# Optimization experiments

Measured on AMD Instinct MI355X. Metric: run time of the kernel, lower is better.

## Reference

```python
import jax, jax.numpy as jnp
import numpy as np

T = 0.07          # cfg.CAP.TEMP
K = 50            # cfg.CAP.HARD_NEG_K
LOSS_WEIGHT = 0.5 # cfg.CAP.LOSS_WEIGHT
C_CAM = 8         # number of cameras
P = 2048          # pseudo-ID classes per camera bank


def setup_inputs() -> dict:
    key = jax.random.key(0)
    k1, k2, k3, k4 = jax.random.split(key, 4)
    B, D = 256, 2048
    inputs = jax.random.normal(k1, (B, D), jnp.float32)
    labels = jax.random.randint(k2, (B,), 0, P)
    cams = jax.random.randint(k3, (B,), 0, C_CAM)
    tempV = jax.random.normal(k4, (C_CAM * P, D), jnp.float32)
    tempV = tempV / jnp.linalg.norm(tempV, axis=1, keepdims=True)  # memory rows are L2-normalized
    return {"inputs": inputs, "labels": labels, "cams": cams, "tempV": tempV}


def _seg_mean_sum(vals, cams):
    # original loops over unique cams: loss += mean(vals within cam); empty cams contribute 0
    sums = jax.ops.segment_sum(vals, cams, num_segments=C_CAM)
    cnts = jax.ops.segment_sum(jnp.ones_like(vals), cams, num_segments=C_CAM)
    return jnp.sum(jnp.where(cnts > 0, sums / jnp.maximum(cnts, 1.0), 0.0))


def reference(inputs, labels, cams, tempV):
    B = inputs.shape[0]
    # cfg.CAP.NORM_FEAT
    x = inputs / jnp.linalg.norm(inputs, axis=1, keepdims=True)

    # one fused matmul against the concatenated memory; per-camera banks are contiguous P-slices
    all_logits = x @ tempV.T                      # [B, C_CAM*P]
    logits3 = all_logits.reshape(B, C_CAM, P)

    # ---- intra-camera loss: logits against the sample's own camera bank ----
    percam = jnp.take_along_axis(logits3, cams[:, None, None], axis=1)[:, 0, :] / T  # [B, P]
    lse_i = jax.scipy.special.logsumexp(percam, axis=1)
    ce = lse_i - jnp.take_along_axis(percam, labels[:, None], axis=1)[:, 0]
    loss_intra = _seg_mean_sum(ce, cams)

    # ---- inter-camera loss with hard-negative mining ----
    rows = jnp.arange(B)[:, None]
    # each ID has one centroid in every camera bank: positions label + P*cam
    ori_ind = labels[:, None] + P * jnp.arange(C_CAM)[None, :]        # [B, C_CAM]
    sims = all_logits.at[rows, ori_ind].set(-10000.0)                 # mask positives
    _, sel_ind = jax.lax.top_k(sims, K)                               # hard negatives (== sort[-K:])
    ori_logits = jnp.take_along_axis(all_logits, ori_ind, axis=1) / T  # [B, C_CAM]
    sel_logits = jnp.take_along_axis(all_logits, sel_ind, axis=1) / T  # [B, K]
    cat = jnp.concatenate([ori_logits, sel_logits], axis=1)            # [B, C_CAM+K]
    lse_c = jax.scipy.special.logsumexp(cat, axis=1)
    # target = 1/len(ori) on positives, 0 on negatives -> lse - mean(positive logits)
    loss_k = lse_c - jnp.mean(ori_logits, axis=1)
    loss_inter = LOSS_WEIGHT * _seg_mean_sum(loss_k, cams)

    return (loss_intra, loss_inter)
```

## Files before the change

kernel.cpp:

```cpp
#include <hip/hip_runtime.h>
#include <hip/hip_bf16.h>

#define BATCH 256
#define DIM   2048
#define NMEM  16384
#define PCLS  2048
#define CCAM  8
#define KSEL  50
#define T_INV 14.285714285714285714f
#define NBIN  4096

typedef __bf16 bf16x8 __attribute__((ext_vector_type(8)));
typedef float  f32x4  __attribute__((ext_vector_type(4)));

static __device__ __forceinline__ unsigned int f2bf(float f) {
  unsigned int u = __float_as_uint(f);
  return (u + 0x7FFFu + ((u >> 16) & 1u)) >> 16;
}
static __device__ __forceinline__ unsigned int pk2(float lo, float hi) {
  return f2bf(lo) | (f2bf(hi) << 16);
}
static __device__ __forceinline__ int binof(float v) {
  float bf = fmaf(v, 1950.4762f, 2048.0f);
  bf = fminf(fmaxf(bf, 0.0f), 4095.0f);
  return (int)bf;
}

__global__ __launch_bounds__(256) void norm_cast_kernel(
    const float* __restrict__ in, unsigned short* __restrict__ xb) {
  __shared__ float red[256];
  const int b = blockIdx.x, t = threadIdx.x;
  const float4* row = (const float4*)(in + (size_t)b * DIM);
  float4 a0 = row[t];
  float4 a1 = row[t + 256];
  float ss = a0.x*a0.x + a0.y*a0.y + a0.z*a0.z + a0.w*a0.w
           + a1.x*a1.x + a1.y*a1.y + a1.z*a1.z + a1.w*a1.w;
  red[t] = ss; __syncthreads();
  for (int s = 128; s > 0; s >>= 1) { if (t < s) red[t] += red[t + s]; __syncthreads(); }
  const float rn = rsqrtf(red[0]);
  ushort4 o0, o1;
  o0.x = (unsigned short)f2bf(a0.x*rn); o0.y = (unsigned short)f2bf(a0.y*rn);
  o0.z = (unsigned short)f2bf(a0.z*rn); o0.w = (unsigned short)f2bf(a0.w*rn);
  o1.x = (unsigned short)f2bf(a1.x*rn); o1.y = (unsigned short)f2bf(a1.y*rn);
  o1.z = (unsigned short)f2bf(a1.z*rn); o1.w = (unsigned short)f2bf(a1.w*rn);
  *(ushort4*)&xb[(size_t)b * DIM + t * 4]         = o0;
  *(ushort4*)&xb[(size_t)b * DIM + (t + 256) * 4] = o1;
}

#define BM 128
#define BN 64
#define BK 64
#define LDT 72

__global__ __launch_bounds__(256, 2) void gemm_kernel(
    const unsigned short* __restrict__ X,
    const float* __restrict__ V,
    float* __restrict__ C) {
  __shared__ unsigned short As[BM * LDT];
  __shared__ unsigned short Bs[BN * LDT];
  const int t  = threadIdx.x;
  const int m0 = blockIdx.x * BM;
  const int n0 = blockIdx.y * BN;
  const int lane = t & 63;
  const int w    = t >> 6;
  const int wm   = (w >> 1) * 64;
  const int wn   = (w & 1) * 32;

  f32x4 acc[4][2];
#pragma unroll
  for (int i = 0; i < 4; i++)
#pragma unroll
    for (int j = 0; j < 2; j++) acc[i][j] = (f32x4){0.f, 0.f, 0.f, 0.f};

  const int sr = t >> 1;
  const int sh = (t & 1) * 32;
  const int rb = t >> 2;
  const int cb = (t & 3) * 16;
  const unsigned short* Xp = X + (size_t)(m0 + sr) * DIM + sh;
  const float*          Vp = V + (size_t)(n0 + rb) * DIM + cb;

  uint4  a0 = *(const uint4*)Xp;
  uint4  a1 = *(const uint4*)(Xp + 8);
  uint4  a2 = *(const uint4*)(Xp + 16);
  uint4  a3 = *(const uint4*)(Xp + 24);
  float4 b0 = *(const float4*)Vp;
  float4 b1 = *(const float4*)(Vp + 4);
  float4 b2 = *(const float4*)(Vp + 8);
  float4 b3 = *(const float4*)(Vp + 12);

  const int fr = lane & 15;
  const int fk = (lane >> 4) * 8;

  for (int k0 = 0; k0 < DIM; k0 += BK) {
    __syncthreads();
    *(uint4*)&As[sr * LDT + sh]      = a0;
    *(uint4*)&As[sr * LDT + sh + 8]  = a1;
    *(uint4*)&As[sr * LDT + sh + 16] = a2;
    *(uint4*)&As[sr * LDT + sh + 24] = a3;
    uint4 p0, p1;
    p0.x = pk2(b0.x, b0.y); p0.y = pk2(b0.z, b0.w);
    p0.z = pk2(b1.x, b1.y); p0.w = pk2(b1.z, b1.w);
    p1.x = pk2(b2.x, b2.y); p1.y = pk2(b2.z, b2.w);
    p1.z = pk2(b3.x, b3.y); p1.w = pk2(b3.z, b3.w);
    *(uint4*)&Bs[rb * LDT + cb]     = p0;
    *(uint4*)&Bs[rb * LDT + cb + 8] = p1;
    __syncthreads();

    if (k0 + BK < DIM) {
      a0 = *(const uint4*)(Xp + k0 + BK);
      a1 = *(const uint4*)(Xp + k0 + BK + 8);
      a2 = *(const uint4*)(Xp + k0 + BK + 16);
      a3 = *(const uint4*)(Xp + k0 + BK + 24);
      b0 = *(const float4*)(Vp + k0 + BK);
      b1 = *(const float4*)(Vp + k0 + BK + 4);
      b2 = *(const float4*)(Vp + k0 + BK + 8);
      b3 = *(const float4*)(Vp + k0 + BK + 12);
    }

#pragma unroll
    for (int kk = 0; kk < BK; kk += 32) {
      bf16x8 aF[4], bF[2];
#pragma unroll
      for (int i = 0; i < 4; i++)
        aF[i] = *(const bf16x8*)&As[(wm + i * 16 + fr) * LDT + kk + fk];
#pragma unroll
      for (int j = 0; j < 2; j++)
        bF[j] = *(const bf16x8*)&Bs[(wn + j * 16 + fr) * LDT + kk + fk];
#pragma unroll
      for (int i = 0; i < 4; i++)
#pragma unroll
        for (int j = 0; j < 2; j++)
          acc[i][j] = __builtin_amdgcn_mfma_f32_16x16x32_bf16(aF[i], bF[j], acc[i][j], 0, 0, 0);
    }
  }

  const int cr = (lane >> 4) * 4;
  const int cc = lane & 15;
#pragma unroll
  for (int i = 0; i < 4; i++)
#pragma unroll
    for (int j = 0; j < 2; j++)
#pragma unroll
      for (int r = 0; r < 4; r++)
        C[(size_t)(m0 + wm + i * 16 + cr + r) * NMEM + (n0 + wn + j * 16 + cc)] =
            acc[i][j][r];
}

__global__ __launch_bounds__(256) void row_loss_kernel(
    const float* __restrict__ logits,
    const int* __restrict__ labels, const int* __restrict__ cams,
    float* __restrict__ ce_out, float* __restrict__ lossk_out) {
  __shared__ float vals[NMEM];
  __shared__ int   hist[NBIN];
  __shared__ float red[256];
  __shared__ int   pint[256];
  __shared__ float bl[512];
  __shared__ int   bcount;
  __shared__ int   bstar_s, cabove_s;

  const int b = blockIdx.x, t = threadIdx.x;
  const float4* src = (const float4*)(logits + (size_t)b * NMEM);
#pragma unroll
  for (int i = 0; i < 16; i++) ((float4*)vals)[t + 256 * i] = src[t + 256 * i];
#pragma unroll
  for (int i = 0; i < NBIN / 256; i++) hist[t + 256 * i] = 0;
  if (t == 0) bcount = 0;
  const int cam = cams[b], label = labels[b];
  __syncthreads();

  const int s0 = cam * PCLS;
  float S = 0.f;
#pragma unroll
  for (int i = 0; i < 8; i++) S += __expf(vals[s0 + t + 256 * i] * T_INV);
  red[t] = S; __syncthreads();
  for (int s = 128; s > 0; s >>= 1) { if (t < s) red[t] += red[t + s]; __syncthreads(); }
  float ov[CCAM]; float sumo = 0.f;
  if (t == 0) {
    ce_out[b] = logf(red[0]) - vals[s0 + label] * T_INV;
#pragma unroll
    for (int c = 0; c < CCAM; c++) { ov[c] = vals[c * PCLS + label]; sumo += ov[c]; }
  }
  __syncthreads();
  if (t < CCAM) vals[t * PCLS + label] = -1e30f;
  __syncthreads();

#pragma unroll
  for (int i = 0; i < 64; i++) {
    int bin = binof(vals[t + 256 * i]);
    atomicAdd(&hist[bin], 1);
  }
  __syncthreads();

  int ps = 0;
#pragma unroll
  for (int i = 0; i < 16; i++) ps += hist[t * 16 + i];
  pint[t] = ps; __syncthreads();
  if (t == 0) {
    int cum = 0, bstar = 0, cab = 0;
    for (int tc = 255; tc >= 0; tc--) {
      if (cum + pint[tc] >= KSEL) {
        for (int bi = tc * 16 + 15; bi >= tc * 16; bi--) {
          int h = hist[bi];
          if (cum + h >= KSEL) { bstar = bi; cab = cum; break; }
          cum += h;
        }
        break;
      }
      cum += pint[tc];
    }
    bstar_s = bstar; cabove_s = cab;
  }
  __syncthreads();
  const int bstar = bstar_s;

  float S2 = 0.f;
#pragma unroll
  for (int i = 0; i < 64; i++) {
    float v = vals[t + 256 * i];
    int bin = binof(v);
    if (bin > bstar) S2 += __expf(v * T_INV);
    else if (bin == bstar) {
      int p = atomicAdd(&bcount, 1);
      if (p < 512) bl[p] = v;
    }
  }
  red[t] = S2; __syncthreads();
  for (int s = 128; s > 0; s >>= 1) { if (t < s) red[t] += red[t + s]; __syncthreads(); }

  if (t == 0) {
    float S2tot = red[0];
    int need = KSEL - cabove_s;
    int bc = min(bcount, 512);
    for (int r = 0; r < need; r++) {
      float mx = -1e30f; int mi = 0;
      for (int i = 0; i < bc; i++) if (bl[i] > mx) { mx = bl[i]; mi = i; }
      S2tot += __expf(mx * T_INV);
      bl[mi] = -1e30f;
    }
#pragma unroll
    for (int c = 0; c < CCAM; c++) S2tot += __expf(ov[c] * T_INV);
    lossk_out[b] = logf(S2tot) - (sumo * T_INV) * (1.0f / CCAM);
  }
}

__global__ __launch_bounds__(256) void finalize_kernel(
    const float* __restrict__ ce, const float* __restrict__ lossk,
    const int* __restrict__ cams, float* __restrict__ out) {
  __shared__ float ce_s[BATCH], lk_s[BATCH];
  __shared__ int   cam_s[BATCH];
  __shared__ float si[CCAM], sk[CCAM], cnt[CCAM];
  const int t = threadIdx.x;
  ce_s[t]  = ce[t];
  lk_s[t]  = lossk[t];
  cam_s[t] = cams[t];
  __syncthreads();
  if (t < CCAM) {
    float a = 0.f, b = 0.f; int n = 0;
    for (int i = 0; i < BATCH; i++) {
      if (cam_s[i] == t) { a += ce_s[i]; b += lk_s[i]; n++; }
    }
    si[t] = a; sk[t] = b; cnt[t] = (float)n;
  }
  __syncthreads();
  if (t == 0) {
    float li = 0.f, lk = 0.f;
    for (int c = 0; c < CCAM; c++) {
      if (cnt[c] > 0.f) { li += si[c] / cnt[c]; lk += sk[c] / cnt[c]; }
    }
    out[0] = li;
    out[1] = 0.5f * lk;
  }
}

extern "C" void kernel_launch(void* const* d_in, const int* in_sizes, int n_in,
                              void* d_out, int out_size, void* d_ws, size_t ws_size,
                              hipStream_t stream) {
  const float* inputs = (const float*)d_in[0];
  const int*   labels = (const int*)d_in[1];
  const int*   cams   = (const int*)d_in[2];
  const float* tempV  = (const float*)d_in[3];
  float* out = (float*)d_out;

  char* ws = (char*)d_ws;
  unsigned short* xb  = (unsigned short*)ws;
  float* logits       = (float*)(ws + (1u << 20));
  float* ce           = (float*)(ws + (1u << 20) + (16u << 20));
  float* lossk        = (float*)(ws + (1u << 20) + (16u << 20) + 1024);

  norm_cast_kernel<<<BATCH, 256, 0, stream>>>(inputs, xb);
  gemm_kernel<<<dim3(BATCH / BM, NMEM / BN), 256, 0, stream>>>(xb, tempV, logits);
  row_loss_kernel<<<BATCH, 256, 0, stream>>>(logits, labels, cams, ce, lossk);
  finalize_kernel<<<1, 256, 0, stream>>>(ce, lossk, cams, out);
}
```

Before: 270.3 us.

## Shrink GEMM N-tile and double-buffer global prefetch in registers

Halves the GEMM block's N tile from 64 to 32 and remaps warps so each computes a 32x32 sub-tile. Occupancy hint rises to 4 blocks per CU, and the grid doubles in the N direction. The K loop now holds two stages of global loads in registers so loads run further ahead of the MFMA work. The cost is more redundant X-tile loads across N-blocks, fewer MFMAs per shared-memory read, and extra syncs per iteration.

```diff
diff --git a/kernel.cpp b/kernel.cpp
--- a/kernel.cpp
+++ b/kernel.cpp
@@ -48,11 +48,11 @@
 }
 
 #define BM 128
-#define BN 64
+#define BN 32
 #define BK 64
 #define LDT 72
 
-__global__ __launch_bounds__(256, 2) void gemm_kernel(
+__global__ __launch_bounds__(256, 4) void gemm_kernel(
     const unsigned short* __restrict__ X,
     const float* __restrict__ V,
     float* __restrict__ C) {
@@ -63,86 +63,106 @@
   const int n0 = blockIdx.y * BN;
   const int lane = t & 63;
   const int w    = t >> 6;
-  const int wm   = (w >> 1) * 64;
-  const int wn   = (w & 1) * 32;
-
-  f32x4 acc[4][2];
-#pragma unroll
-  for (int i = 0; i < 4; i++)
+  const int wm   = w * 32;
+
+  f32x4 acc[2][2];
+#pragma unroll
+  for (int i = 0; i < 2; i++)
 #pragma unroll
     for (int j = 0; j < 2; j++) acc[i][j] = (f32x4){0.f, 0.f, 0.f, 0.f};
 
-  const int sr = t >> 1;
-  const int sh = (t & 1) * 32;
-  const int rb = t >> 2;
-  const int cb = (t & 3) * 16;
-  const unsigned short* Xp = X + (size_t)(m0 + sr) * DIM + sh;
-  const float*          Vp = V + (size_t)(n0 + rb) * DIM + cb;
-
-  uint4  a0 = *(const uint4*)Xp;
-  uint4  a1 = *(const uint4*)(Xp + 8);
-  uint4  a2 = *(const uint4*)(Xp + 16);
-  uint4  a3 = *(const uint4*)(Xp + 24);
-  float4 b0 = *(const float4*)Vp;
-  float4 b1 = *(const float4*)(Vp + 4);
-  float4 b2 = *(const float4*)(Vp + 8);
-  float4 b3 = *(const float4*)(Vp + 12);
+  const int ar = t >> 3;
+  const int ac = (t & 7) * 8;
+  const int br = t >> 4;
+  const int bc = (t & 15) * 4;
+  const unsigned short* Xp = X + (size_t)(m0 + ar) * DIM + ac;
+  const float*          Vp = V + (size_t)(n0 + br) * DIM + bc;
+
+  uint4  A0[4], A1[4];
+  float4 B0[2], B1[2];
+#pragma unroll
+  for (int j = 0; j < 4; j++) A0[j] = *(const uint4*)(Xp + j * 32 * DIM);
+#pragma unroll
+  for (int j = 0; j < 2; j++) B0[j] = *(const float4*)(Vp + j * 16 * DIM);
+#pragma unroll
+  for (int j = 0; j < 4; j++) A1[j] = *(const uint4*)(Xp + j * 32 * DIM + BK);
+#pragma unroll
+  for (int j = 0; j < 2; j++) B1[j] = *(const float4*)(Vp + j * 16 * DIM + BK);
 
   const int fr = lane & 15;
   const int fk = (lane >> 4) * 8;
 
-  for (int k0 = 0; k0 < DIM; k0 += BK) {
+  for (int k0 = 0; k0 < DIM; k0 += 2 * BK) {
     __syncthreads();
-    *(uint4*)&As[sr * LDT + sh]      = a0;
-    *(uint4*)&As[sr * LDT + sh + 8]  = a1;
-    *(uint4*)&As[sr * LDT + sh + 16] = a2;
-    *(uint4*)&As[sr * LDT + sh + 24] = a3;
-    uint4 p0, p1;
-    p0.x = pk2(b0.x, b0.y); p0.y = pk2(b0.z, b0.w);
-    p0.z = pk2(b1.x, b1.y); p0.w = pk2(b1.z, b1.w);
-    p1.x = pk2(b2.x, b2.y); p1.y = pk2(b2.z, b2.w);
-    p1.z = pk2(b3.x, b3.y); p1.w = pk2(b3.z, b3.w);
-    *(uint4*)&Bs[rb * LDT + cb]     = p0;
-    *(uint4*)&Bs[rb * LDT + cb + 8] = p1;
+#pragma unroll
+    for (int j = 0; j < 4; j++)
+      *(uint4*)&As[(ar + 32 * j) * LDT + ac] = A0[j];
+#pragma unroll
+    for (int j = 0; j < 2; j++) {
+      uint2 p; p.x = pk2(B0[j].x, B0[j].y); p.y = pk2(B0[j].z, B0[j].w);
+      *(uint2*)&Bs[(br + 16 * j) * LDT + bc] = p;
+    }
+    if (k0 + 2 * BK < DIM) {
+#pragma unroll
+      for (int j = 0; j < 4; j++)
+        A0[j] = *(const uint4*)(Xp + j * 32 * DIM + k0 + 2 * BK);
+#pragma unroll
+      for (int j = 0; j < 2; j++)
+        B0[j] = *(const float4*)(Vp + j * 16 * DIM + k0 + 2 * BK);
+    }
     __syncthreads();
-
-    if (k0 + BK < DIM) {
-      a0 = *(const uint4*)(Xp + k0 + BK);
-      a1 = *(const uint4*)(Xp + k0 + BK + 8);
-      a2 = *(const uint4*)(Xp + k0 + BK + 16);
-      a3 = *(const uint4*)(Xp + k0 + BK + 24);
-      b0 = *(const float4*)(Vp + k0 + BK);
-      b1 = *(const float4*)(Vp + k0 + BK + 4);
-      b2 = *(const float4*)(Vp + k0 + BK + 8);
-      b3 = *(const float4*)(Vp + k0 + BK + 12);
-    }
-
 #pragma unroll
     for (int kk = 0; kk < BK; kk += 32) {
-      bf16x8 aF[4], bF[2];
-#pragma unroll
-      for (int i = 0; i < 4; i++)
-        aF[i] = *(const bf16x8*)&As[(wm + i * 16 + fr) * LDT + kk + fk];
+      bf16x8 aF0 = *(const bf16x8*)&As[(wm +      fr) * LDT + kk + fk];
+      bf16x8 aF1 = *(const bf16x8*)&As[(wm + 16 + fr) * LDT + kk + fk];
+      bf16x8 bF0 = *(const bf16x8*)&Bs[(          fr) * LDT + kk + fk];
+      bf16x8 bF1 = *(const bf16x8*)&Bs[(     16 + fr) * LDT + kk + fk];
+      acc[0][0] = __builtin_amdgcn_mfma_f32_16x16x32_bf16(aF0, bF0, acc[0][0], 0, 0, 0);
+      acc[0][1] = __builtin_amdgcn_mfma_f32_16x16x32_bf16(aF0, bF1, acc[0][1], 0, 0, 0);
+      acc[1][0] = __builtin_amdgcn_mfma_f32_16x16x32_bf16(aF1, bF0, acc[1][0], 0, 0, 0);
+      acc[1][1] = __builtin_amdgcn_mfma_f32_16x16x32_bf16(aF1, bF1, acc[1][1], 0, 0, 0);
+    }
+
+    __syncthreads();
+#pragma unroll
+    for (int j = 0; j < 4; j++)
+      *(uint4*)&As[(ar + 32 * j) * LDT + ac] = A1[j];
+#pragma unroll
+    for (int j = 0; j < 2; j++) {
+      uint2 p; p.x = pk2(B1[j].x, B1[j].y); p.y = pk2(B1[j].z, B1[j].w);
+      *(uint2*)&Bs[(br + 16 * j) * LDT + bc] = p;
+    }
+    if (k0 + 3 * BK < DIM) {
+#pragma unroll
+      for (int j = 0; j < 4; j++)
+        A1[j] = *(const uint4*)(Xp + j * 32 * DIM + k0 + 3 * BK);
 #pragma unroll
       for (int j = 0; j < 2; j++)
-        bF[j] = *(const bf16x8*)&Bs[(wn + j * 16 + fr) * LDT + kk + fk];
-#pragma unroll
-      for (int i = 0; i < 4; i++)
-#pragma unroll
-        for (int j = 0; j < 2; j++)
-          acc[i][j] = __builtin_amdgcn_mfma_f32_16x16x32_bf16(aF[i], bF[j], acc[i][j], 0, 0, 0);
+        B1[j] = *(const float4*)(Vp + j * 16 * DIM + k0 + 3 * BK);
+    }
+    __syncthreads();
+#pragma unroll
+    for (int kk = 0; kk < BK; kk += 32) {
+      bf16x8 aF0 = *(const bf16x8*)&As[(wm +      fr) * LDT + kk + fk];
+      bf16x8 aF1 = *(const bf16x8*)&As[(wm + 16 + fr) * LDT + kk + fk];
+      bf16x8 bF0 = *(const bf16x8*)&Bs[(          fr) * LDT + kk + fk];
+      bf16x8 bF1 = *(const bf16x8*)&Bs[(     16 + fr) * LDT + kk + fk];
+      acc[0][0] = __builtin_amdgcn_mfma_f32_16x16x32_bf16(aF0, bF0, acc[0][0], 0, 0, 0);
+      acc[0][1] = __builtin_amdgcn_mfma_f32_16x16x32_bf16(aF0, bF1, acc[0][1], 0, 0, 0);
+      acc[1][0] = __builtin_amdgcn_mfma_f32_16x16x32_bf16(aF1, bF0, acc[1][0], 0, 0, 0);
+      acc[1][1] = __builtin_amdgcn_mfma_f32_16x16x32_bf16(aF1, bF1, acc[1][1], 0, 0, 0);
     }
   }
 
   const int cr = (lane >> 4) * 4;
   const int cc = lane & 15;
 #pragma unroll
-  for (int i = 0; i < 4; i++)
+  for (int i = 0; i < 2; i++)
 #pragma unroll
     for (int j = 0; j < 2; j++)
 #pragma unroll
       for (int r = 0; r < 4; r++)
-        C[(size_t)(m0 + wm + i * 16 + cr + r) * NMEM + (n0 + wn + j * 16 + cc)] =
+        C[(size_t)(m0 + wm + i * 16 + cr + r) * NMEM + (n0 + j * 16 + cc)] =
             acc[i][j][r];
 }
 
```

After: 436.7 us. 61.6% more time.
